# Kernel tuning notes

Hardware: AMD Instinct MI355X
Metric: run time of the kernel (lower is better)

## Reference

```python
import jax, jax.numpy as jnp
import numpy as np

T, B, OBS, H, A = 256, 128, 512, 1024, 18


def setup_inputs() -> dict:
    key = jax.random.key(0)
    ks = jax.random.split(key, 9)
    s = 0.02
    return {
        "state": jax.random.normal(ks[0], (T, B, OBS), dtype=jnp.float32),
        "mask": jax.random.randint(ks[1], (T, B), 0, 2, dtype=jnp.int32),
        "W_enc": jax.random.normal(ks[2], (H, OBS), dtype=jnp.float32) * s,
        "b_enc": jnp.zeros((H,), dtype=jnp.float32),
        "W_ih": jax.random.normal(ks[3], (4 * H, H), dtype=jnp.float32) * s,
        "W_hh": jax.random.normal(ks[4], (4 * H, H), dtype=jnp.float32) * s,
        "b_ih": jnp.zeros((4 * H,), dtype=jnp.float32),
        "b_hh": jnp.zeros((4 * H,), dtype=jnp.float32),
        "W_dec": jax.random.normal(ks[5], (A, H), dtype=jnp.float32) * s,
        "b_dec": jnp.zeros((A,), dtype=jnp.float32),
    }


def reference(state, mask, W_enc, b_enc, W_ih, W_hh, b_ih, b_hh, W_dec, b_dec):
    maskf = mask.astype(state.dtype)  # (T, B)
    hidden = W_hh.shape[1]
    # encode all timesteps in one GEMM: (T,B,OBS) @ (OBS,H)
    encoded = jax.nn.relu(jnp.einsum('tbo,ho->tbh', state, W_enc) + b_enc)
    # precompute input contribution to all gates (T,B,4H)
    x_gates = jnp.einsum('tbh,gh->tbg', encoded, W_ih) + b_ih + b_hh
    h0 = jnp.zeros((state.shape[1], hidden), dtype=state.dtype)
    c0 = jnp.zeros_like(h0)

    def step(carry, inp):
        h, c = carry
        xg, m = inp  # xg: (B,4H), m: (B,)
        gates = xg + h @ W_hh.T
        i, f, g, o = jnp.split(gates, 4, axis=-1)  # PyTorch LSTMCell gate order
        i = jax.nn.sigmoid(i)
        f = jax.nn.sigmoid(f)
        g = jnp.tanh(g)
        o = jax.nn.sigmoid(o)
        c_new = (f * c + i * g) * m[:, None]
        h_new = (o * jnp.tanh(f * c + i * g)) * m[:, None]
        return (h_new, c_new), h_new

    (h, c), latent = jax.lax.scan(step, (h0, c0), (x_gates, maskf))
    # decode all timesteps in one GEMM, then apply mask
    values = jnp.einsum('tbh,ah->tba', latent, W_dec) + b_dec
    values = values * maskf[:, :, None]
    return values, h, c
```

## Files before the change

kernel.cpp:

```cpp
#include <hip/hip_runtime.h>

#define T_STEPS 256
#define BATCH   128
#define OBSD    512
#define HID     1024
#define GH      4096
#define ACTD    18
#define TBROWS  (T_STEPS*BATCH)
#define NWG     256
#define JG      16

typedef __bf16 bf16x8_t __attribute__((ext_vector_type(8)));
typedef float  f32x4_t  __attribute__((ext_vector_type(4)));

__device__ __forceinline__ ushort f2bf(float f) {
  unsigned u = __builtin_bit_cast(unsigned, f);
  u += 0x7fffu + ((u >> 16) & 1u);
  return (ushort)(u >> 16);
}
__device__ __forceinline__ float bf2f(ushort s) {
  return __builtin_bit_cast(float, ((unsigned)s) << 16);
}
__device__ __forceinline__ f32x4_t mfma16(bf16x8_t a, bf16x8_t b, f32x4_t c) {
  return __builtin_amdgcn_mfma_f32_16x16x32_bf16(a, b, c, 0, 0, 0);
}
__device__ __forceinline__ void gl_lds16(const void* g, void* l) {
  __builtin_amdgcn_global_load_lds(
      (__attribute__((address_space(1))) void*)(g),
      (__attribute__((address_space(3))) void*)(l), 16, 0, 0);
}
__device__ __forceinline__ float sigm(float x) { return 1.f / (1.f + __expf(-x)); }
__device__ __forceinline__ float tanhf_fast(float x) {
  float e = __expf(2.f * x);
  return (e - 1.f) / (e + 1.f);
}
__device__ __forceinline__ void wait_vm0() { __builtin_amdgcn_s_waitcnt(0x0F70); }

__global__ void cast_bf16_kernel(const float* __restrict__ in, ushort* __restrict__ out, int n4) {
  int i = blockIdx.x * blockDim.x + threadIdx.x;
  int stride = gridDim.x * blockDim.x;
  for (; i < n4; i += stride) {
    float4 v = reinterpret_cast<const float4*>(in)[i];
    ushort4 o;
    o.x = f2bf(v.x); o.y = f2bf(v.y); o.z = f2bf(v.z); o.w = f2bf(v.w);
    reinterpret_cast<ushort4*>(out)[i] = o;
  }
}

__global__ void cast_permute_wih_kernel(const float* __restrict__ in, ushort* __restrict__ out) {
  int idx = blockIdx.x * 256 + threadIdx.x;
  int rowd = idx >> 7;
  int c8 = (idx & 127) << 3;
  int g = rowd & 3, hid = rowd >> 2;
  const float* src = in + ((size_t)g * HID + hid) * HID + c8;
  ushort* dst = out + (size_t)rowd * HID + c8;
#pragma unroll
  for (int i = 0; i < 8; ++i) dst[i] = f2bf(src[i]);
}

__global__ void bias_perm_kernel(const float* __restrict__ bih, const float* __restrict__ bhh,
                                 float* __restrict__ out) {
  int i = blockIdx.x * 256 + threadIdx.x;
  int g = i & 3, hid = i >> 2;
  out[i] = bih[g * HID + hid] + bhh[g * HID + hid];
}

__global__ __launch_bounds__(256) void gemm_bt_kernel(
    const ushort* __restrict__ A, const ushort* __restrict__ Bt,
    const float* __restrict__ bias1,
    ushort* __restrict__ C, int M, int N, int K, int relu,
    const int* __restrict__ omask, float* __restrict__ ovals)
{
  __shared__ ushort la[128 * 64];
  __shared__ ushort lb[128 * 64];

  const int tid  = threadIdx.x;
  const int lane = tid & 63;
  const int w    = tid >> 6;
  const int wm   = w >> 1, wn = w & 1;
  const int nwg = gridDim.x;
  const int q8  = nwg >> 3;
  const int bid = (blockIdx.x & 7) * q8 + (blockIdx.x >> 3);
  const int ntiles = N >> 7;
  const int bm = bid / ntiles, bn = bid % ntiles;
  const size_t m0 = (size_t)bm << 7, n0 = (size_t)bn << 7;

  const int lrow = lane & 15;
  const int lk   = (lane >> 4) << 3;
  const int wavebase = (tid & ~63);

  f32x4_t acc[4][4];
  const f32x4_t zero = {0.f, 0.f, 0.f, 0.f};
#pragma unroll
  for (int i = 0; i < 4; ++i)
#pragma unroll
    for (int j = 0; j < 4; ++j) acc[i][j] = zero;

  for (int k0 = 0; k0 < K; k0 += 64) {
#pragma unroll
    for (int p = 0; p < 4; ++p) {
      int c = p * 256 + tid;
      int r = c >> 3;
      int q = (c & 7) << 3;
      gl_lds16(A + (m0 + r) * (size_t)K + k0 + q, la + (size_t)(p * 256 + wavebase) * 8);
      gl_lds16(Bt + (n0 + r) * (size_t)K + k0 + q, lb + (size_t)(p * 256 + wavebase) * 8);
    }
    __syncthreads();
#pragma unroll
    for (int kk = 0; kk < 64; kk += 32) {
      bf16x8_t af[4], bfr[4];
#pragma unroll
      for (int i = 0; i < 4; ++i)
        af[i] = *(const bf16x8_t*)(la + (wm * 64 + i * 16 + lrow) * 64 + kk + lk);
#pragma unroll
      for (int j = 0; j < 4; ++j)
        bfr[j] = *(const bf16x8_t*)(lb + (wn * 64 + j * 16 + lrow) * 64 + kk + lk);
#pragma unroll
      for (int i = 0; i < 4; ++i)
#pragma unroll
        for (int j = 0; j < 4; ++j)
          acc[i][j] = mfma16(af[i], bfr[j], acc[i][j]);
    }
    __syncthreads();
  }

  const int crow0 = (lane >> 4) * 4;
  if (ovals) {
#pragma unroll
    for (int j = 0; j < 4; ++j) {
      int col = wn * 64 + j * 16 + lrow;
      if (col < ACTD) {
        float bv = bias1[col];
#pragma unroll
        for (int i = 0; i < 4; ++i) {
#pragma unroll
          for (int r = 0; r < 4; ++r) {
            size_t row = m0 + wm * 64 + i * 16 + crow0 + r;
            float mv = (float)omask[row];
            ovals[row * ACTD + col] = (acc[i][j][r] + bv) * mv;
          }
        }
      }
    }
    return;
  }
#pragma unroll
  for (int j = 0; j < 4; ++j) {
    int col = (int)n0 + wn * 64 + j * 16 + lrow;
    float bv = bias1 ? bias1[col] : 0.f;
#pragma unroll
    for (int i = 0; i < 4; ++i) {
#pragma unroll
      for (int r = 0; r < 4; ++r) {
        size_t row = m0 + wm * 64 + i * 16 + crow0 + r;
        float v = acc[i][j][r] + bv;
        if (relu) v = fmaxf(v, 0.f);
        C[row * (size_t)N + col] = f2bf(v);
      }
    }
  }
}

__global__ __launch_bounds__(256, 1) void lstm_scan_kernel(
    const ushort* __restrict__ xg,
    const ushort* __restrict__ whh,
    const int* __restrict__ mask,
    const ushort* __restrict__ hinit,
    ushort* __restrict__ hseq,
    float* __restrict__ cbuf,
    float* __restrict__ outh, float* __restrict__ outc,
    unsigned* __restrict__ flags,
    int t0, int nsteps)
{
  __shared__ __align__(16) ushort lds_pool[64 * 1024];
  __shared__ __align__(16) ushort hexch[32 * 16];

  const int tid  = threadIdx.x;
  const int lane = tid & 63;
  const int w    = tid >> 6;
  const int wg   = blockIdx.x;
  const int bq   = wg >> 6;
  const int jg   = wg & 63;
  const int j0   = jg * JG;
  const int b0   = bq * 32;

  const int lrow = lane & 15;
  const int lkg  = lane >> 4;

  for (int c = tid; c < 64 * 128; c += 256) {
    int r = c >> 7, gn = c & 127;
    int jj = r >> 2, g = r & 3;
    const ushort* src = whh + ((size_t)g * HID + j0 + jj) * HID + gn * 8;
    int gnd = (gn & ~7) | ((gn & 7) ^ (r & 7));
    *reinterpret_cast<uint4*>(&lds_pool[r * 1024 + gnd * 8]) =
        *reinterpret_cast<const uint4*>(src);
  }
  __syncthreads();

  bf16x8_t af[8][4];
#pragma unroll
  for (int kc = 0; kc < 8; ++kc) {
#pragma unroll
    for (int ks = 0; ks < 4; ++ks) {
      int gA = kc * 16 + ks * 4 + lkg;
      int gAs = (gA & ~7) | ((gA & 7) ^ (lrow & 7));
      af[kc][ks] = *(const bf16x8_t*)(lds_pool + (size_t)(w * 16 + lrow) * 1024 + gAs * 8);
    }
  }
  __syncthreads();
  ushort* hstg = lds_pool;

  const int jjc = w * 4 + lkg;
  const int bl0 = lrow, bl1 = 16 + lrow;

  float creg0, creg1;
  if (t0 == 0) { creg0 = creg1 = 0.f; }
  else {
    creg0 = cbuf[(size_t)(b0 + bl0) * HID + j0 + jjc];
    creg1 = cbuf[(size_t)(b0 + bl1) * HID + j0 + jjc];
  }

  const int s0 = w * 128 + lane;
  const int s1 = s0 + 64;
  const int sb0 = s0 >> 4, sq0 = s0 & 15;
  const int sb1 = s1 >> 4, sq1 = s1 & 15;
  const int gg0 = (sq0 & 8) | ((sq0 & 7) ^ (sb0 & 7));
  const int gg1 = (sq1 & 8) | ((sq1 & 7) ^ (sb1 & 7));

  const unsigned* fpoll = &flags[(size_t)(bq * 64 + lane) * 16];

  ushort4 xv0, xv1;
  float m0v, m1v;
  {
    xv0 = *(const ushort4*)(xg + (size_t)(b0 + bl0) * GH + (j0 + jjc) * 4);
    xv1 = *(const ushort4*)(xg + (size_t)(b0 + bl1) * GH + (j0 + jjc) * 4);
    m0v = (float)mask[b0 + bl0];
    m1v = (float)mask[b0 + bl1];
  }
  __builtin_amdgcn_sched_barrier(0);

#define CHUNK(KC, VN) do {                                                     \
    __builtin_amdgcn_s_waitcnt(0x0F70 | (VN));                                 \
    __builtin_amdgcn_s_barrier();                                              \
    __builtin_amdgcn_sched_barrier(0);                                         \
    const ushort* sbuf = hstg + (size_t)(KC) * 4096;                           \
    _Pragma("unroll")                                                          \
    for (int ks = 0; ks < 4; ++ks) {                                           \
      int q16 = ks * 4 + lkg;                                                  \
      int qs = (q16 & 8) | ((q16 & 7) ^ (bl0 & 7));                            \
      bf16x8_t bf0 = *(const bf16x8_t*)(sbuf + (size_t)bl0 * 128 + qs * 8);    \
      bf16x8_t bf1 = *(const bf16x8_t*)(sbuf + (size_t)bl1 * 128 + qs * 8);    \
      acc0 = mfma16(af[KC][ks], bf0, acc0);                                    \
      acc1 = mfma16(af[KC][ks], bf1, acc1);                                    \
    }                                                                          \
    __builtin_amdgcn_sched_barrier(0);                                         \
  } while (0)

  for (int tl = 0; tl < nsteps; ++tl) {
    const ushort* hsrc = (t0 + tl == 0)
        ? (hinit + (size_t)b0 * HID)
        : (hseq + (size_t)(t0 + tl - 1) * (BATCH * HID) + (size_t)b0 * HID);

    wait_vm0();
    __builtin_amdgcn_sched_barrier(0);

    f32x4_t acc0 = {0.f, 0.f, 0.f, 0.f};
    f32x4_t acc1 = {0.f, 0.f, 0.f, 0.f};

#pragma unroll
    for (int kc = 0; kc < 8; ++kc) {
      gl_lds16(hsrc + (size_t)sb0 * HID + (kc * 16 + gg0) * 8,
               hstg + (size_t)kc * 4096 + (size_t)(w * 128) * 8);
      gl_lds16(hsrc + (size_t)sb1 * HID + (kc * 16 + gg1) * 8,
               hstg + (size_t)kc * 4096 + (size_t)(w * 128 + 64) * 8);
    }
    __builtin_amdgcn_sched_barrier(0);

    CHUNK(0, 14); CHUNK(1, 12); CHUNK(2, 10); CHUNK(3, 8);
    CHUNK(4, 6);  CHUNK(5, 4);  CHUNK(6, 2);  CHUNK(7, 0);

    {
      float ig = sigm(acc0[0] + bf2f(xv0.x));
      float fg = sigm(acc0[1] + bf2f(xv0.y));
      float gt = tanhf_fast(acc0[2] + bf2f(xv0.z));
      float og = sigm(acc0[3] + bf2f(xv0.w));
      float cp = fg * creg0 + ig * gt;
      creg0 = cp * m0v;
      float h0 = og * tanhf_fast(cp) * m0v;

      ig = sigm(acc1[0] + bf2f(xv1.x));
      fg = sigm(acc1[1] + bf2f(xv1.y));
      gt = tanhf_fast(acc1[2] + bf2f(xv1.z));
      og = sigm(acc1[3] + bf2f(xv1.w));
      cp = fg * creg1 + ig * gt;
      creg1 = cp * m1v;
      float h1 = og * tanhf_fast(cp) * m1v;

      ushort hb0 = f2bf(h0), hb1 = f2bf(h1);
      hexch[bl0 * 16 + jjc] = hb0;
      hexch[bl1 * 16 + jjc] = hb1;
      if (t0 + tl == T_STEPS - 1) {
        outh[(size_t)(b0 + bl0) * HID + j0 + jjc] = h0;
        outh[(size_t)(b0 + bl1) * HID + j0 + jjc] = h1;
        outc[(size_t)(b0 + bl0) * HID + j0 + jjc] = creg0;
        outc[(size_t)(b0 + bl1) * HID + j0 + jjc] = creg1;
      }
    }
    __syncthreads();

    if (tid < 128) {
      int bl = tid >> 2, seg = tid & 3;
      unsigned long long v = *(const unsigned long long*)(&hexch[bl * 16 + seg * 4]);
      unsigned long long* dst = (unsigned long long*)(hseq +
          (size_t)(t0 + tl) * (BATCH * HID) + (size_t)(b0 + bl) * HID + j0 + seg * 4);
      __hip_atomic_store(dst, v, __ATOMIC_RELAXED, __HIP_MEMORY_SCOPE_AGENT);
    }

    if (tl != nsteps - 1) {
      __syncthreads();
      const unsigned tgt = (unsigned)(t0 + tl + 1);
      if (tid == 0)
        __hip_atomic_store(&flags[(size_t)wg * 16], tgt, __ATOMIC_RELAXED, __HIP_MEMORY_SCOPE_AGENT);
      {
        const ushort* xp = xg + (size_t)(tl + 1) * BATCH * GH;
        xv0 = *(const ushort4*)(xp + (size_t)(b0 + bl0) * GH + (j0 + jjc) * 4);
        xv1 = *(const ushort4*)(xp + (size_t)(b0 + bl1) * GH + (j0 + jjc) * 4);
        m0v = (float)mask[(tl + 1) * BATCH + b0 + bl0];
        m1v = (float)mask[(tl + 1) * BATCH + b0 + bl1];
      }
      __builtin_amdgcn_sched_barrier(0);
      if (tid < 64) {
        for (;;) {
          unsigned v = __hip_atomic_load(fpoll, __ATOMIC_RELAXED, __HIP_MEMORY_SCOPE_AGENT);
          if (__all(v >= tgt)) break;
        }
      }
      __syncthreads();
    }
  }
#undef CHUNK

  cbuf[(size_t)(b0 + bl0) * HID + j0 + jjc] = creg0;
  cbuf[(size_t)(b0 + bl1) * HID + j0 + jjc] = creg1;
}

extern "C" void kernel_launch(void* const* d_in, const int* in_sizes, int n_in,
                              void* d_out, int out_size, void* d_ws, size_t ws_size,
                              hipStream_t stream) {
  (void)in_sizes; (void)n_in; (void)out_size;
  const float* state = (const float*)d_in[0];
  const int*   mask  = (const int*)d_in[1];
  const float* Wenc  = (const float*)d_in[2];
  const float* benc  = (const float*)d_in[3];
  const float* Wih   = (const float*)d_in[4];
  const float* Whh   = (const float*)d_in[5];
  const float* bih   = (const float*)d_in[6];
  const float* bhh   = (const float*)d_in[7];
  const float* Wdec  = (const float*)d_in[8];
  const float* bdec  = (const float*)d_in[9];

  float* out_values = (float*)d_out;
  float* out_h = out_values + (size_t)TBROWS * ACTD;
  float* out_c = out_h + (size_t)BATCH * HID;

  auto pad256 = [](size_t b) { return (b + 255) & ~(size_t)255; };

  const size_t sz_wenc  = (size_t)HID * OBSD * 2;
  const size_t sz_wih   = (size_t)GH * HID * 2;
  const size_t sz_whh   = (size_t)GH * HID * 2;
  const size_t sz_wdec  = (size_t)128 * HID * 2;
  const size_t sz_bdec  = 512;
  const size_t sz_bperm = (size_t)GH * sizeof(float);
  const size_t sz_flags = NWG * 16 * sizeof(unsigned);
  const size_t sz_hseq  = (size_t)TBROWS * HID * 2;
  const size_t sz_hinit = (size_t)BATCH * HID * 2;
  const size_t sz_cbuf  = (size_t)BATCH * HID * 4;
  const size_t fixed = pad256(sz_wenc) + pad256(sz_wih) + pad256(sz_whh) +
                       pad256(sz_wdec) + pad256(sz_bdec) + pad256(sz_bperm) +
                       pad256(sz_flags) + pad256(sz_hseq) + pad256(sz_hinit) +
                       pad256(sz_cbuf);

  int Tc = 8;
  {
    const int cands[6] = {256, 128, 64, 32, 16, 8};
    for (int ci = 0; ci < 6; ++ci) {
      int tc = cands[ci];
      size_t per = pad256((size_t)tc * BATCH * HID * 2)
                 + pad256((size_t)tc * BATCH * GH * 2);
      if (fixed + per <= ws_size) { Tc = tc; break; }
    }
  }
  const int nchunks = T_STEPS / Tc;
  const int crows = Tc * BATCH;

  char* ws = (char*)d_ws;
  size_t off = 0;
  auto alloc = [&](size_t b) { char* r = ws + off; off += pad256(b); return r; };
  ushort* wenc_bf  = (ushort*)alloc(sz_wenc);
  ushort* wih_perm = (ushort*)alloc(sz_wih);
  ushort* whh_bf   = (ushort*)alloc(sz_whh);
  ushort* wdec_pad = (ushort*)alloc(sz_wdec);
  float*  bdec_pad = (float*)alloc(sz_bdec);
  float*  bperm    = (float*)alloc(sz_bperm);
  unsigned* flags  = (unsigned*)alloc(sz_flags);
  ushort* hseq     = (ushort*)alloc(sz_hseq);
  ushort* hinit    = (ushort*)alloc(sz_hinit);
  float*  cbuf     = (float*)alloc(sz_cbuf);
  ushort* enc_c    = (ushort*)alloc((size_t)crows * HID * 2);
  ushort* xg_c     = (ushort*)alloc((size_t)crows * GH * 2);
  ushort* state_c  = xg_c;

  hipMemsetAsync(hinit, 0, sz_hinit, stream);
  hipMemsetAsync(flags, 0, sz_flags, stream);
  hipMemsetAsync(wdec_pad, 0, sz_wdec, stream);
  hipMemsetAsync(bdec_pad, 0, sz_bdec, stream);
  hipMemcpyAsync(bdec_pad, bdec, ACTD * sizeof(float), hipMemcpyDeviceToDevice, stream);

  auto cast = [&](const float* src, ushort* dst, size_t n) {
    int n4 = (int)(n / 4);
    int blocks = (n4 + 255) / 256;
    if (blocks > 4096) blocks = 4096;
    cast_bf16_kernel<<<blocks, 256, 0, stream>>>(src, dst, n4);
  };
  cast(Wenc, wenc_bf, (size_t)HID * OBSD);
  cast(Whh, whh_bf, (size_t)GH * HID);
  cast(Wdec, wdec_pad, (size_t)ACTD * HID);
  cast_permute_wih_kernel<<<(GH * 128) / 256, 256, 0, stream>>>(Wih, wih_perm);
  bias_perm_kernel<<<GH / 256, 256, 0, stream>>>(bih, bhh, bperm);

  for (int c = 0; c < nchunks; ++c) {
    const int t0 = c * Tc;
    cast(state + (size_t)t0 * BATCH * OBSD, state_c, (size_t)crows * OBSD);
    gemm_bt_kernel<<<(crows / 128) * (HID / 128), 256, 0, stream>>>(
        state_c, wenc_bf, benc, enc_c, crows, HID, OBSD, 1, nullptr, nullptr);
    gemm_bt_kernel<<<(crows / 128) * (GH / 128), 256, 0, stream>>>(
        enc_c, wih_perm, bperm, xg_c, crows, GH, HID, 0, nullptr, nullptr);
    lstm_scan_kernel<<<NWG, 256, 0, stream>>>(
        xg_c, whh_bf, mask + (size_t)t0 * BATCH, hinit, hseq, cbuf,
        out_h, out_c, flags, t0, Tc);
  }

  gemm_bt_kernel<<<TBROWS / 128, 256, 0, stream>>>(
      hseq, wdec_pad, bdec_pad, nullptr, TBROWS, 128, HID, 0,
      mask, out_values);
}
```

Baseline: 1.546 ms.

## Add 256x256-tile double-buffered bf16 GEMM for encoder and input-gate projections

Adds a new GEMM kernel with 256x256 output tiles, 512 threads, and a double-buffered LDS pipeline. It stages tiles with direct global-to-LDS loads into a swizzled layout and remaps the grid in an XCD-aware order. The encoder and input-gate GEMMs now use it in place of the 128-tile kernel, to raise arithmetic intensity and overlap loads with MFMA. The trade-offs are higher register and LDS use and the requirement that M and N be multiples of 256, with the grid remap assuming a block count divisible by 8.

```diff
diff --git a/kernel.cpp b/kernel.cpp
--- a/kernel.cpp
+++ b/kernel.cpp
@@ -34,6 +34,7 @@
   float e = __expf(2.f * x);
   return (e - 1.f) / (e + 1.f);
 }
+#define WAITVM(N) __builtin_amdgcn_s_waitcnt(0x0F70 | ((N) & 15))
 __device__ __forceinline__ void wait_vm0() { __builtin_amdgcn_s_waitcnt(0x0F70); }
 
 __global__ void cast_bf16_kernel(const float* __restrict__ in, ushort* __restrict__ out, int n4) {
@@ -154,6 +155,109 @@
       for (int r = 0; r < 4; ++r) {
         size_t row = m0 + wm * 64 + i * 16 + crow0 + r;
         float v = acc[i][j][r] + bv;
+        if (relu) v = fmaxf(v, 0.f);
+        C[row * (size_t)N + col] = f2bf(v);
+      }
+    }
+  }
+}
+
+__global__ __launch_bounds__(512, 2) void gemm256_kernel(
+    const ushort* __restrict__ A, const ushort* __restrict__ Bt,
+    const float* __restrict__ bias,
+    ushort* __restrict__ C, int M, int N, int K, int relu)
+{
+  __shared__ __align__(16) ushort lds[2][2][16384];
+
+  const int tid  = threadIdx.x;
+  const int lane = tid & 63;
+  const int wid  = tid >> 6;
+  const int wm   = wid >> 2, wn = wid & 3;
+  const int nwg  = gridDim.x;
+  const int q8   = nwg >> 3;
+  const int bid  = (blockIdx.x & 7) * q8 + (blockIdx.x >> 3);
+  const int ntiles = N >> 8;
+  const int bm = bid / ntiles, bn = bid % ntiles;
+  const size_t m0 = (size_t)bm << 8, n0 = (size_t)bn << 8;
+
+  const int lrow = lane & 15;
+  const int lkg  = lane >> 4;
+
+  int srow[4], sgsr[4];
+#pragma unroll
+  for (int q = 0; q < 4; ++q) {
+    int s = (q * 8 + wid) * 64 + lane;
+    srow[q] = s >> 3;
+    sgsr[q] = (s & 7) ^ ((s >> 3) & 7);
+  }
+
+#define STAGE256(BUF, KT) do {                                                \
+    const size_t kb_ = (size_t)(KT) * 64;                                     \
+    _Pragma("unroll")                                                         \
+    for (int q = 0; q < 4; ++q) {                                             \
+      gl_lds16(A  + (m0 + srow[q]) * (size_t)K + kb_ + sgsr[q] * 8,           \
+               &lds[BUF][0][(q * 8 + wid) * 512]);                            \
+      gl_lds16(Bt + (n0 + srow[q]) * (size_t)K + kb_ + sgsr[q] * 8,           \
+               &lds[BUF][1][(q * 8 + wid) * 512]);                            \
+    }                                                                         \
+  } while (0)
+
+  f32x4_t acc[8][4];
+  const f32x4_t zero = {0.f, 0.f, 0.f, 0.f};
+#pragma unroll
+  for (int f = 0; f < 8; ++f)
+#pragma unroll
+    for (int n = 0; n < 4; ++n) acc[f][n] = zero;
+
+  const int nkt = K >> 6;
+  STAGE256(0, 0);
+  STAGE256(1, 1);
+
+  for (int kt = 0; kt < nkt; ++kt) {
+    const int buf = kt & 1;
+    if (kt + 1 < nkt) WAITVM(8); else WAITVM(0);
+    __builtin_amdgcn_s_barrier();
+    __builtin_amdgcn_sched_barrier(0);
+#pragma unroll
+    for (int p = 0; p < 4; ++p) {
+      const int kk = p >> 1, mg = p & 1;
+      bf16x8_t av[4], bv[4];
+#pragma unroll
+      for (int f = 0; f < 4; ++f) {
+        int ar = wm * 128 + (mg * 4 + f) * 16 + lrow;
+        int ags = (kk * 4 + lkg) ^ (ar & 7);
+        av[f] = *(const bf16x8_t*)&lds[buf][0][ar * 64 + ags * 8];
+      }
+#pragma unroll
+      for (int n = 0; n < 4; ++n) {
+        int br = wn * 64 + n * 16 + lrow;
+        int bgs = (kk * 4 + lkg) ^ (br & 7);
+        bv[n] = *(const bf16x8_t*)&lds[buf][1][br * 64 + bgs * 8];
+      }
+      __builtin_amdgcn_s_setprio(1);
+#pragma unroll
+      for (int f = 0; f < 4; ++f)
+#pragma unroll
+        for (int n = 0; n < 4; ++n)
+          acc[mg * 4 + f][n] = mfma16(av[f], bv[n], acc[mg * 4 + f][n]);
+      __builtin_amdgcn_s_setprio(0);
+    }
+    __builtin_amdgcn_s_barrier();
+    if (kt + 2 < nkt) STAGE256(buf, kt + 2);
+  }
+#undef STAGE256
+
+  const int crow0 = lkg * 4;
+#pragma unroll
+  for (int n = 0; n < 4; ++n) {
+    int col = (int)n0 + wn * 64 + n * 16 + lrow;
+    float bvv = bias ? bias[col] : 0.f;
+#pragma unroll
+    for (int f = 0; f < 8; ++f) {
+#pragma unroll
+      for (int r = 0; r < 4; ++r) {
+        size_t row = m0 + (size_t)wm * 128 + f * 16 + crow0 + r;
+        float v = acc[f][n][r] + bvv;
         if (relu) v = fmaxf(v, 0.f);
         C[row * (size_t)N + col] = f2bf(v);
       }
@@ -431,10 +535,10 @@
   for (int c = 0; c < nchunks; ++c) {
     const int t0 = c * Tc;
     cast(state + (size_t)t0 * BATCH * OBSD, state_c, (size_t)crows * OBSD);
-    gemm_bt_kernel<<<(crows / 128) * (HID / 128), 256, 0, stream>>>(
-        state_c, wenc_bf, benc, enc_c, crows, HID, OBSD, 1, nullptr, nullptr);
-    gemm_bt_kernel<<<(crows / 128) * (GH / 128), 256, 0, stream>>>(
-        enc_c, wih_perm, bperm, xg_c, crows, GH, HID, 0, nullptr, nullptr);
+    gemm256_kernel<<<(crows / 256) * (HID / 256), 512, 0, stream>>>(
+        state_c, wenc_bf, benc, enc_c, crows, HID, OBSD, 1);
+    gemm256_kernel<<<(crows / 256) * (GH / 256), 512, 0, stream>>>(
+        enc_c, wih_perm, bperm, xg_c, crows, GH, HID, 0);
     lstm_scan_kernel<<<NWG, 256, 0, stream>>>(
         xg_c, whh_bf, mask + (size_t)t0 * BATCH, hinit, hseq, cbuf,
         out_h, out_c, flags, t0, Tc);
```

Measured after the change: 1.417 ms. -8.4%, faster.
